# Optimization experiments

Hardware: AMD Instinct MI355X
Metric: run time of the kernel (lower is better)

Reference implementation:

```python
import jax, jax.numpy as jnp
import numpy as np

B, C_IN, N = 8, 32, 400000


def setup_inputs() -> dict:
    key = jax.random.key(0)
    ks = jax.random.split(key, 7)
    X = jax.random.normal(ks[0], (B, C_IN, N), dtype=jnp.float32)
    # 1x1 Conv1d weights == per-point linear layers: [out_ch, in_ch] + bias [out_ch]
    W1 = jax.random.normal(ks[1], (16, 32), dtype=jnp.float32) * (1.0 / np.sqrt(32))
    b1 = jax.random.normal(ks[2], (16,), dtype=jnp.float32) * 0.01
    W2 = jax.random.normal(ks[3], (8, 16), dtype=jnp.float32) * (1.0 / np.sqrt(16))
    b2 = jax.random.normal(ks[4], (8,), dtype=jnp.float32) * 0.01
    W3 = jax.random.normal(ks[5], (1, 8), dtype=jnp.float32) * (1.0 / np.sqrt(8))
    b3 = jax.random.normal(ks[6], (1,), dtype=jnp.float32) * 0.01
    return {"X": X, "K": 64, "W1": W1, "b1": b1, "W2": W2, "b2": b2, "W3": W3, "b3": b3}


def reference(X, K, W1, b1, W2, b2, W3, b3):
    # fc1: 1x1 conv (32->16) + ReLU
    h = jax.nn.relu(jnp.einsum('oc,bcn->bon', W1, X) + b1[None, :, None])
    # fc2: 1x1 conv (16->8) + ReLU
    h = jax.nn.relu(jnp.einsum('oc,bcn->bon', W2, h) + b2[None, :, None])
    # fc3: 1x1 conv (8->1) + Softplus -> scores [B, 1, N]
    s = jax.nn.softplus(jnp.einsum('oc,bcn->bon', W3, h) + b3[None, :, None])
    # top-K along last dim (largest, sorted -- matches torch.topk defaults)
    _, idx = jax.lax.top_k(s, K)  # [B, 1, K]
    return idx.reshape(-1)
```

## Files before the change

kernel.cpp:

```cpp
#include <hip/hip_runtime.h>
#include <math.h>

#define NPTS 400000
#define NBATCH 8
#define K_OUT 64
#define IDX_SENTINEL 0x7fffffff

#define WB_W2 512
#define WB_B1 640
#define WB_B2 656
#define WB_W3 664
#define WB_B3 672

__device__ __forceinline__ bool better(float av, int ai, float bv, int bi) {
    return (av > bv) || (av == bv && ai < bi);
}

__device__ __forceinline__ void cmp_swap(float& v, int& i, int j, bool keepBetter) {
    float ov = __shfl_xor(v, j);
    int   oi = __shfl_xor(i, j);
    bool ob = better(ov, oi, v, i);
    if (keepBetter ? ob : !ob) { v = ov; i = oi; }
}

__device__ __forceinline__ void wave_topk_insert(float& bv, int& bi, float nv, int ni, int lane) {
    float tv = __shfl(bv, 63);
    int   ti = __shfl(bi, 63);
    if (__ballot(better(nv, ni, tv, ti)) == 0ULL) return;
#pragma unroll
    for (int k = 2; k <= 64; k <<= 1) {
#pragma unroll
        for (int j = k >> 1; j > 0; j >>= 1) {
            bool keepBetter = (((lane & k) == 0) == ((lane & j) == 0));
            cmp_swap(nv, ni, j, keepBetter);
        }
    }
    float rv = __shfl(nv, lane ^ 63);
    int   ri = __shfl(ni, lane ^ 63);
    if (better(rv, ri, bv, bi)) { bv = rv; bi = ri; }
#pragma unroll
    for (int j = 32; j > 0; j >>= 1) cmp_swap(bv, bi, j, (lane & j) == 0);
}

__global__ __launch_bounds__(256) void prep_weights(
    const float* __restrict__ W1, const float* __restrict__ b1,
    const float* __restrict__ W2, const float* __restrict__ b2,
    const float* __restrict__ W3, const float* __restrict__ b3,
    float* __restrict__ wbuf)
{
    int t = threadIdx.x;
    for (int i = t; i < 512; i += 256) wbuf[i] = W1[(i & 15) * 32 + (i >> 4)];
    if (t < 128) wbuf[WB_W2 + t] = W2[(t & 7) * 16 + (t >> 3)];
    if (t < 16)       wbuf[WB_B1 + t] = b1[t];
    else if (t < 24)  wbuf[WB_B2 + (t - 16)] = b2[t - 16];
    else if (t < 32)  wbuf[WB_W3 + (t - 24)] = W3[t - 24];
    else if (t == 32) wbuf[WB_B3] = b3[0];
}

__global__ __launch_bounds__(256, 4) void mlp_score_topk_k1(
    const float* __restrict__ X, const float* __restrict__ wb,
    int2* __restrict__ cand, int ppw)
{
    int t = threadIdx.x;
    int b = blockIdx.y;
    int wave = blockIdx.x * 4 + (t >> 6);
    int lane = t & 63;
    const float* Xb = X + (size_t)b * 32 * NPTS;

    float bv = -INFINITY;
    int   bi = IDX_SENTINEL;

    int riters = ppw >> 8;
    int waveStart = wave * ppw;

#pragma unroll 1
    for (int r = 0; r < riters; ++r) {
        int n = waveStart + r * 256 + lane * 4;
        float z0 = -INFINITY, z1 = -INFINITY, z2 = -INFINITY, z3 = -INFINITY;
        bool valid = (n < NPTS);
        if (valid) {
            float4 a1[16];
#pragma unroll
            for (int o = 0; o < 16; ++o) a1[o] = make_float4(0.f, 0.f, 0.f, 0.f);
#pragma unroll
            for (int cb = 0; cb < 8; ++cb) {
                float4 x[4];
#pragma unroll
                for (int j = 0; j < 4; ++j)
                    x[j] = *reinterpret_cast<const float4*>(Xb + (size_t)(cb * 4 + j) * NPTS + n);
#pragma unroll
                for (int j = 0; j < 4; ++j) {
                    int c = cb * 4 + j;
#pragma unroll
                    for (int o = 0; o < 16; ++o) {
                        float w = wb[c * 16 + o];
                        a1[o].x = fmaf(w, x[j].x, a1[o].x);
                        a1[o].y = fmaf(w, x[j].y, a1[o].y);
                        a1[o].z = fmaf(w, x[j].z, a1[o].z);
                        a1[o].w = fmaf(w, x[j].w, a1[o].w);
                    }
                }
            }
            float4 a2[8];
#pragma unroll
            for (int o = 0; o < 8; ++o) a2[o] = make_float4(0.f, 0.f, 0.f, 0.f);
#pragma unroll
            for (int c = 0; c < 16; ++c) {
                float bb = wb[WB_B1 + c];
                float4 h = a1[c];
                h.x = fmaxf(h.x + bb, 0.f);
                h.y = fmaxf(h.y + bb, 0.f);
                h.z = fmaxf(h.z + bb, 0.f);
                h.w = fmaxf(h.w + bb, 0.f);
#pragma unroll
                for (int o = 0; o < 8; ++o) {
                    float w = wb[WB_W2 + c * 8 + o];
                    a2[o].x = fmaf(w, h.x, a2[o].x);
                    a2[o].y = fmaf(w, h.y, a2[o].y);
                    a2[o].z = fmaf(w, h.z, a2[o].z);
                    a2[o].w = fmaf(w, h.w, a2[o].w);
                }
            }
            float4 zacc = make_float4(0.f, 0.f, 0.f, 0.f);
#pragma unroll
            for (int c = 0; c < 8; ++c) {
                float bb = wb[WB_B2 + c];
                float4 h = a2[c];
                h.x = fmaxf(h.x + bb, 0.f);
                h.y = fmaxf(h.y + bb, 0.f);
                h.z = fmaxf(h.z + bb, 0.f);
                h.w = fmaxf(h.w + bb, 0.f);
                float w = wb[WB_W3 + c];
                zacc.x = fmaf(w, h.x, zacc.x);
                zacc.y = fmaf(w, h.y, zacc.y);
                zacc.z = fmaf(w, h.z, zacc.z);
                zacc.w = fmaf(w, h.w, zacc.w);
            }
            float b3v = wb[WB_B3];
            z0 = zacc.x + b3v; z1 = zacc.y + b3v; z2 = zacc.z + b3v; z3 = zacc.w + b3v;
        }
        int i0 = valid ? (n + 0) : IDX_SENTINEL;
        int i1 = valid ? (n + 1) : IDX_SENTINEL;
        int i2 = valid ? (n + 2) : IDX_SENTINEL;
        int i3 = valid ? (n + 3) : IDX_SENTINEL;
        wave_topk_insert(bv, bi, z0, i0, lane);
        wave_topk_insert(bv, bi, z1, i1, lane);
        wave_topk_insert(bv, bi, z2, i2, lane);
        wave_topk_insert(bv, bi, z3, i3, lane);
    }

    cand[((size_t)b * gridDim.x * 4 + wave) * 64 + lane] = make_int2(__float_as_int(bv), bi);
}

__global__ __launch_bounds__(256) void topk_merge_k2a(
    const int2* __restrict__ cand, int2* __restrict__ cand2, int lpb)
{
    __shared__ int2 sbuf[4 * 64];
    int b = blockIdx.y;
    int bk = blockIdx.x;
    int t = threadIdx.x;
    int w = t >> 6, lane = t & 63;
    const int2* cb = cand + (size_t)b * lpb * 64;

    float bv = -INFINITY;
    int   bi = IDX_SENTINEL;
    int slot = bk * 4 + w;
#pragma unroll 1
    for (int L = slot; L < lpb; L += 64) {
        int2 p = cb[(size_t)L * 64 + lane];
        wave_topk_insert(bv, bi, __int_as_float(p.x), p.y, lane);
    }
    sbuf[w * 64 + lane] = make_int2(__float_as_int(bv), bi);
    __syncthreads();

    if (w == 0) {
#pragma unroll 1
        for (int q = 1; q < 4; ++q) {
            int2 p = sbuf[q * 64 + lane];
            wave_topk_insert(bv, bi, __int_as_float(p.x), p.y, lane);
        }
        cand2[((size_t)b * 16 + bk) * 64 + lane] = make_int2(__float_as_int(bv), bi);
    }
}

__global__ __launch_bounds__(256) void topk_merge_k2b(
    const int2* __restrict__ cand2, int* __restrict__ out)
{
    __shared__ int2 sbuf[4 * 64];
    int b = blockIdx.x;
    int t = threadIdx.x;
    int w = t >> 6, lane = t & 63;
    const int2* cb = cand2 + (size_t)b * 16 * 64;

    int2 p0 = cb[(size_t)(w * 4) * 64 + lane];
    float bv = __int_as_float(p0.x);
    int   bi = p0.y;
#pragma unroll 1
    for (int q = 1; q < 4; ++q) {
        int2 p = cb[(size_t)(w * 4 + q) * 64 + lane];
        wave_topk_insert(bv, bi, __int_as_float(p.x), p.y, lane);
    }
    sbuf[w * 64 + lane] = make_int2(__float_as_int(bv), bi);
    __syncthreads();

    if (w == 0) {
#pragma unroll 1
        for (int q = 1; q < 4; ++q) {
            int2 p = sbuf[q * 64 + lane];
            wave_topk_insert(bv, bi, __int_as_float(p.x), p.y, lane);
        }
        out[b * K_OUT + lane] = bi;
    }
}

extern "C" void kernel_launch(void* const* d_in, const int* in_sizes, int n_in,
                              void* d_out, int out_size, void* d_ws, size_t ws_size,
                              hipStream_t stream) {
    const float* X  = (const float*)d_in[0];
    const float* W1 = (const float*)d_in[2];
    const float* b1 = (const float*)d_in[3];
    const float* W2 = (const float*)d_in[4];
    const float* b2 = (const float*)d_in[5];
    const float* W3 = (const float*)d_in[6];
    const float* b3 = (const float*)d_in[7];

    int ppw = 256;
    int bx, lpb;
    for (;;) {
        int wpb = (NPTS + ppw - 1) / ppw;
        bx = (wpb + 3) / 4;
        lpb = bx * 4;
        size_t need = 4096
                    + (size_t)NBATCH * lpb * 64 * sizeof(int2)
                    + (size_t)NBATCH * 16 * 64 * sizeof(int2);
        if (need <= ws_size || ppw >= NPTS) break;
        ppw += 256;
    }

    float* wbuf = (float*)d_ws;
    int2*  cand = (int2*)((char*)d_ws + 4096);
    int2*  cand2 = cand + (size_t)NBATCH * lpb * 64;
    int*   out  = (int*)d_out;

    prep_weights<<<1, 256, 0, stream>>>(W1, b1, W2, b2, W3, b3, wbuf);
    mlp_score_topk_k1<<<dim3(bx, NBATCH), 256, 0, stream>>>(X, wbuf, cand, ppw);
    topk_merge_k2a<<<dim3(16, NBATCH), 256, 0, stream>>>(cand, cand2, lpb);
    topk_merge_k2b<<<dim3(NBATCH), 256, 0, stream>>>(cand2, out);
}
```

Measured before the change: 191.4 us.

## Split MLP scoring from top-k scan and add quad-max early reject

Unfuses the scoring kernel. A pure streaming MLP kernel now writes all scores to a workspace buffer, and a separate scan kernel runs the per-wave top-k insertion over fixed 4096-point chunks. The scan first tests the maximum of each lane's four scores against the current 64th-best and skips all four inserts when no lane qualifies. This separates the bandwidth-bound MLP from the shuffle-heavy top-k, in exchange for an extra 12.8 MB score write and re-read and one more launch. It also drops the workspace-size fallback logic, so it assumes the workspace is large enough.

```diff
diff --git a/kernel.cpp b/kernel.cpp
--- a/kernel.cpp
+++ b/kernel.cpp
@@ -2,9 +2,14 @@
 #include <math.h>
 
 #define NPTS 400000
+#define NQUAD 100000
 #define NBATCH 8
 #define K_OUT 64
 #define IDX_SENTINEL 0x7fffffff
+
+#define PPW2 4096
+#define K2_BLOCKS 25
+#define LPB (K2_BLOCKS * 4)
 
 #define WB_W2 512
 #define WB_B1 640
@@ -57,116 +62,133 @@
     else if (t == 32) wbuf[WB_B3] = b3[0];
 }
 
-__global__ __launch_bounds__(256, 4) void mlp_score_topk_k1(
+__global__ __launch_bounds__(256, 4) void mlp_score_k1(
     const float* __restrict__ X, const float* __restrict__ wb,
-    int2* __restrict__ cand, int ppw)
+    float* __restrict__ z)
+{
+    int q = blockIdx.x * 256 + threadIdx.x;
+    if (q >= NQUAD) return;
+    int b = blockIdx.y;
+    int n = q * 4;
+    const float* Xb = X + (size_t)b * 32 * NPTS;
+
+    float4 a1[16];
+#pragma unroll
+    for (int o = 0; o < 16; ++o) a1[o] = make_float4(0.f, 0.f, 0.f, 0.f);
+#pragma unroll
+    for (int cb = 0; cb < 8; ++cb) {
+        float4 x[4];
+#pragma unroll
+        for (int j = 0; j < 4; ++j)
+            x[j] = *reinterpret_cast<const float4*>(Xb + (size_t)(cb * 4 + j) * NPTS + n);
+#pragma unroll
+        for (int j = 0; j < 4; ++j) {
+            int c = cb * 4 + j;
+#pragma unroll
+            for (int o = 0; o < 16; ++o) {
+                float w = wb[c * 16 + o];
+                a1[o].x = fmaf(w, x[j].x, a1[o].x);
+                a1[o].y = fmaf(w, x[j].y, a1[o].y);
+                a1[o].z = fmaf(w, x[j].z, a1[o].z);
+                a1[o].w = fmaf(w, x[j].w, a1[o].w);
+            }
+        }
+    }
+    float4 a2[8];
+#pragma unroll
+    for (int o = 0; o < 8; ++o) a2[o] = make_float4(0.f, 0.f, 0.f, 0.f);
+#pragma unroll
+    for (int c = 0; c < 16; ++c) {
+        float bb = wb[WB_B1 + c];
+        float4 h = a1[c];
+        h.x = fmaxf(h.x + bb, 0.f);
+        h.y = fmaxf(h.y + bb, 0.f);
+        h.z = fmaxf(h.z + bb, 0.f);
+        h.w = fmaxf(h.w + bb, 0.f);
+#pragma unroll
+        for (int o = 0; o < 8; ++o) {
+            float w = wb[WB_W2 + c * 8 + o];
+            a2[o].x = fmaf(w, h.x, a2[o].x);
+            a2[o].y = fmaf(w, h.y, a2[o].y);
+            a2[o].z = fmaf(w, h.z, a2[o].z);
+            a2[o].w = fmaf(w, h.w, a2[o].w);
+        }
+    }
+    float4 zacc = make_float4(0.f, 0.f, 0.f, 0.f);
+#pragma unroll
+    for (int c = 0; c < 8; ++c) {
+        float bb = wb[WB_B2 + c];
+        float4 h = a2[c];
+        h.x = fmaxf(h.x + bb, 0.f);
+        h.y = fmaxf(h.y + bb, 0.f);
+        h.z = fmaxf(h.z + bb, 0.f);
+        h.w = fmaxf(h.w + bb, 0.f);
+        float w = wb[WB_W3 + c];
+        zacc.x = fmaf(w, h.x, zacc.x);
+        zacc.y = fmaf(w, h.y, zacc.y);
+        zacc.z = fmaf(w, h.z, zacc.z);
+        zacc.w = fmaf(w, h.w, zacc.w);
+    }
+    float b3v = wb[WB_B3];
+    zacc.x += b3v; zacc.y += b3v; zacc.z += b3v; zacc.w += b3v;
+    *reinterpret_cast<float4*>(z + (size_t)b * NPTS + n) = zacc;
+}
+
+__global__ __launch_bounds__(256) void topk_scan_k2(
+    const float* __restrict__ z, int2* __restrict__ cand)
 {
     int t = threadIdx.x;
     int b = blockIdx.y;
     int wave = blockIdx.x * 4 + (t >> 6);
     int lane = t & 63;
-    const float* Xb = X + (size_t)b * 32 * NPTS;
+    const float* zb = z + (size_t)b * NPTS;
 
     float bv = -INFINITY;
     int   bi = IDX_SENTINEL;
-
-    int riters = ppw >> 8;
-    int waveStart = wave * ppw;
-
-#pragma unroll 1
-    for (int r = 0; r < riters; ++r) {
+    int waveStart = wave * PPW2;
+
+#pragma unroll 1
+    for (int r = 0; r < PPW2 / 256; ++r) {
         int n = waveStart + r * 256 + lane * 4;
         float z0 = -INFINITY, z1 = -INFINITY, z2 = -INFINITY, z3 = -INFINITY;
         bool valid = (n < NPTS);
         if (valid) {
-            float4 a1[16];
-#pragma unroll
-            for (int o = 0; o < 16; ++o) a1[o] = make_float4(0.f, 0.f, 0.f, 0.f);
-#pragma unroll
-            for (int cb = 0; cb < 8; ++cb) {
-                float4 x[4];
-#pragma unroll
-                for (int j = 0; j < 4; ++j)
-                    x[j] = *reinterpret_cast<const float4*>(Xb + (size_t)(cb * 4 + j) * NPTS + n);
-#pragma unroll
-                for (int j = 0; j < 4; ++j) {
-                    int c = cb * 4 + j;
-#pragma unroll
-                    for (int o = 0; o < 16; ++o) {
-                        float w = wb[c * 16 + o];
-                        a1[o].x = fmaf(w, x[j].x, a1[o].x);
-                        a1[o].y = fmaf(w, x[j].y, a1[o].y);
-                        a1[o].z = fmaf(w, x[j].z, a1[o].z);
-                        a1[o].w = fmaf(w, x[j].w, a1[o].w);
-                    }
-                }
-            }
-            float4 a2[8];
-#pragma unroll
-            for (int o = 0; o < 8; ++o) a2[o] = make_float4(0.f, 0.f, 0.f, 0.f);
-#pragma unroll
-            for (int c = 0; c < 16; ++c) {
-                float bb = wb[WB_B1 + c];
-                float4 h = a1[c];
-                h.x = fmaxf(h.x + bb, 0.f);
-                h.y = fmaxf(h.y + bb, 0.f);
-                h.z = fmaxf(h.z + bb, 0.f);
-                h.w = fmaxf(h.w + bb, 0.f);
-#pragma unroll
-                for (int o = 0; o < 8; ++o) {
-                    float w = wb[WB_W2 + c * 8 + o];
-                    a2[o].x = fmaf(w, h.x, a2[o].x);
-                    a2[o].y = fmaf(w, h.y, a2[o].y);
-                    a2[o].z = fmaf(w, h.z, a2[o].z);
-                    a2[o].w = fmaf(w, h.w, a2[o].w);
-                }
-            }
-            float4 zacc = make_float4(0.f, 0.f, 0.f, 0.f);
-#pragma unroll
-            for (int c = 0; c < 8; ++c) {
-                float bb = wb[WB_B2 + c];
-                float4 h = a2[c];
-                h.x = fmaxf(h.x + bb, 0.f);
-                h.y = fmaxf(h.y + bb, 0.f);
-                h.z = fmaxf(h.z + bb, 0.f);
-                h.w = fmaxf(h.w + bb, 0.f);
-                float w = wb[WB_W3 + c];
-                zacc.x = fmaf(w, h.x, zacc.x);
-                zacc.y = fmaf(w, h.y, zacc.y);
-                zacc.z = fmaf(w, h.z, zacc.z);
-                zacc.w = fmaf(w, h.w, zacc.w);
-            }
-            float b3v = wb[WB_B3];
-            z0 = zacc.x + b3v; z1 = zacc.y + b3v; z2 = zacc.z + b3v; z3 = zacc.w + b3v;
+            float4 zq = *reinterpret_cast<const float4*>(zb + n);
+            z0 = zq.x; z1 = zq.y; z2 = zq.z; z3 = zq.w;
         }
         int i0 = valid ? (n + 0) : IDX_SENTINEL;
         int i1 = valid ? (n + 1) : IDX_SENTINEL;
         int i2 = valid ? (n + 2) : IDX_SENTINEL;
         int i3 = valid ? (n + 3) : IDX_SENTINEL;
+        float m01 = fmaxf(z0, z1), m23 = fmaxf(z2, z3);
+        float m = fmaxf(m01, m23);
+        float tv = __shfl(bv, 63);
+        int   ti = __shfl(bi, 63);
+        if (__ballot(better(m, i0, tv, ti)) == 0ULL) continue;
         wave_topk_insert(bv, bi, z0, i0, lane);
         wave_topk_insert(bv, bi, z1, i1, lane);
         wave_topk_insert(bv, bi, z2, i2, lane);
         wave_topk_insert(bv, bi, z3, i3, lane);
     }
 
-    cand[((size_t)b * gridDim.x * 4 + wave) * 64 + lane] = make_int2(__float_as_int(bv), bi);
+    cand[((size_t)b * LPB + wave) * 64 + lane] = make_int2(__float_as_int(bv), bi);
 }
 
 __global__ __launch_bounds__(256) void topk_merge_k2a(
-    const int2* __restrict__ cand, int2* __restrict__ cand2, int lpb)
+    const int2* __restrict__ cand, int2* __restrict__ cand2)
 {
     __shared__ int2 sbuf[4 * 64];
     int b = blockIdx.y;
     int bk = blockIdx.x;
     int t = threadIdx.x;
     int w = t >> 6, lane = t & 63;
-    const int2* cb = cand + (size_t)b * lpb * 64;
+    const int2* cb = cand + (size_t)b * LPB * 64;
 
     float bv = -INFINITY;
     int   bi = IDX_SENTINEL;
     int slot = bk * 4 + w;
 #pragma unroll 1
-    for (int L = slot; L < lpb; L += 64) {
+    for (int L = slot; L < LPB; L += 64) {
         int2 p = cb[(size_t)L * 64 + lane];
         wave_topk_insert(bv, bi, __int_as_float(p.x), p.y, lane);
     }
@@ -224,26 +246,15 @@
     const float* W3 = (const float*)d_in[6];
     const float* b3 = (const float*)d_in[7];
 
-    int ppw = 256;
-    int bx, lpb;
-    for (;;) {
-        int wpb = (NPTS + ppw - 1) / ppw;
-        bx = (wpb + 3) / 4;
-        lpb = bx * 4;
-        size_t need = 4096
-                    + (size_t)NBATCH * lpb * 64 * sizeof(int2)
-                    + (size_t)NBATCH * 16 * 64 * sizeof(int2);
-        if (need <= ws_size || ppw >= NPTS) break;
-        ppw += 256;
-    }
-
-    float* wbuf = (float*)d_ws;
-    int2*  cand = (int2*)((char*)d_ws + 4096);
-    int2*  cand2 = cand + (size_t)NBATCH * lpb * 64;
-    int*   out  = (int*)d_out;
+    float* wbuf  = (float*)d_ws;
+    float* zbuf  = (float*)((char*)d_ws + 4096);
+    int2*  cand  = (int2*)((char*)zbuf + (size_t)NBATCH * NPTS * sizeof(float));
+    int2*  cand2 = cand + (size_t)NBATCH * LPB * 64;
+    int*   out   = (int*)d_out;
 
     prep_weights<<<1, 256, 0, stream>>>(W1, b1, W2, b2, W3, b3, wbuf);
-    mlp_score_topk_k1<<<dim3(bx, NBATCH), 256, 0, stream>>>(X, wbuf, cand, ppw);
-    topk_merge_k2a<<<dim3(16, NBATCH), 256, 0, stream>>>(cand, cand2, lpb);
+    mlp_score_k1<<<dim3((NQUAD + 255) / 256, NBATCH), 256, 0, stream>>>(X, wbuf, zbuf);
+    topk_scan_k2<<<dim3(K2_BLOCKS, NBATCH), 256, 0, stream>>>(zbuf, cand);
+    topk_merge_k2a<<<dim3(16, NBATCH), 256, 0, stream>>>(cand, cand2);
     topk_merge_k2b<<<dim3(NBATCH), 256, 0, stream>>>(cand2, out);
 }
```

Result: slower. 240.9 us (+25.9%).
